# Optimization experiments

Hardware: AMD Instinct MI355X
Metric: run time of the kernel (lower is better)

## Reference

```python
import jax, jax.numpy as jnp
import numpy as np

B, T, D, U = 64, 2048, 128, 256


def setup_inputs() -> dict:
    key = jax.random.key(0)
    k1, k2, k3 = jax.random.split(key, 3)
    inputs = jax.random.normal(k1, (B, T, D), dtype=jnp.float32)
    # kernel: Dense(4*units, use_bias=False) -> Wx [D, 4U]
    Wx = jax.random.normal(k2, (D, 4 * U), dtype=jnp.float32) * (1.0 / np.sqrt(D))
    # recurrent_kernel: Dense(4*units) with bias (orthogonal init approximated by scaled normal)
    Wh = jax.random.normal(k3, (U, 4 * U), dtype=jnp.float32) * (1.0 / np.sqrt(U))
    b = jnp.zeros((4 * U,), dtype=jnp.float32)
    return {"inputs": inputs, "Wx": Wx, "Wh": Wh, "b": b}


def reference(inputs, Wx, Wh, b):
    units = Wh.shape[0]
    batch = inputs.shape[0]
    # Precompute input projections for all timesteps: [B, T, 4U]
    xz = jnp.einsum('btd,dk->btk', inputs, Wx)

    def step(carry, xz_t):
        h, c = carry
        z = xz_t + h @ Wh + b  # [B, 4U]
        zi, zf, zg, zo = jnp.split(z, 4, axis=-1)
        i = jax.nn.sigmoid(zi)
        f = jax.nn.sigmoid(zf)
        o = jax.nn.sigmoid(zo)
        c_new = f * c + i * jnp.tanh(zg)
        h_new = o * jnp.tanh(c_new)
        return (h_new, c_new), h_new

    h0 = jnp.zeros((batch, units), dtype=inputs.dtype)
    c0 = jnp.zeros((batch, units), dtype=inputs.dtype)
    # scan over time: xz transposed to [T, B, 4U]
    _, hs = jax.lax.scan(step, (h0, c0), jnp.swapaxes(xz, 0, 1))
    return jnp.swapaxes(hs, 0, 1)  # [B, T, U]
```

## Files before the change

### kernel.cpp

```cpp
#include <hip/hip_runtime.h>
#include <hip/hip_fp16.h>


#define NB 64
#define NT 2048
#define ND 128
#define NU 256
#define N4U 1024

#define WREG 96
#define WLDS 32

typedef _Float16 f16;
typedef _Float16 f16x2 __attribute__((ext_vector_type(2)));
typedef _Float16 f16x8 __attribute__((ext_vector_type(8)));
typedef float f32x4 __attribute__((ext_vector_type(4)));

__device__ __forceinline__ float dot2(f16x2 a, f16x2 b, float c) {
  return __builtin_amdgcn_fdot2(a, b, c, false);
}

__device__ __forceinline__ float sigm(float x) { return 1.0f / (1.0f + __expf(-x)); }
__device__ __forceinline__ float tanh_(float x) { return 1.0f - 2.0f / (__expf(2.0f * x) + 1.0f); }

__global__ __launch_bounds__(256) void xz_gemm(const float* __restrict__ X,
                                               const float* __restrict__ Wx,
                                               float* __restrict__ XZ,
                                               int t0, int tc) {
  __shared__ __align__(16) float xs[64][ND];
  __shared__ __align__(16) float ws[ND][64];
  const int tid = threadIdx.x;
  const int b = blockIdx.y;
  const int row0 = t0 + blockIdx.x * 64;
  const int col0 = blockIdx.z * 64;

  {
    const float* src = X + ((size_t)b * NT + row0) * ND;
#pragma unroll
    for (int ii = 0; ii < 8; ++ii) {
      int q = tid + 256 * ii;
      int r = q >> 5;
      int k4 = q & 31;
      f32x4 v = *(const f32x4*)(src + (size_t)r * ND + 4 * k4);
      *(f32x4*)&xs[r][4 * k4] = v;
    }
#pragma unroll
    for (int ii = 0; ii < 8; ++ii) {
      int q = tid + 256 * ii;
      int k = q >> 4;
      int c4 = q & 15;
      f32x4 v = *(const f32x4*)(Wx + (size_t)k * N4U + col0 + 4 * c4);
      *(f32x4*)&ws[k][4 * c4] = v;
    }
  }
  __syncthreads();

  const int tx = tid & 15, ty = tid >> 4;
  float acc[4][4];
#pragma unroll
  for (int i = 0; i < 4; ++i)
#pragma unroll
    for (int j = 0; j < 4; ++j) acc[i][j] = 0.0f;

#pragma unroll 8
  for (int k = 0; k < ND; ++k) {
    f32x4 bv = *(const f32x4*)&ws[k][4 * tx];
    float a0 = xs[4 * ty + 0][k];
    float a1 = xs[4 * ty + 1][k];
    float a2 = xs[4 * ty + 2][k];
    float a3 = xs[4 * ty + 3][k];
#pragma unroll
    for (int j = 0; j < 4; ++j) {
      acc[0][j] += a0 * bv[j];
      acc[1][j] += a1 * bv[j];
      acc[2][j] += a2 * bv[j];
      acc[3][j] += a3 * bv[j];
    }
  }

  float* dst = XZ + ((size_t)b * tc + (row0 - t0)) * N4U + col0;
#pragma unroll
  for (int i = 0; i < 4; ++i) {
    f32x4 v;
#pragma unroll
    for (int j = 0; j < 4; ++j) v[j] = acc[i][j];
    *(f32x4*)(dst + (size_t)(4 * ty + i) * N4U + 4 * tx) = v;
  }
}

__global__ __launch_bounds__(512, 1) void lstm_seq(const float* __restrict__ Wh,
                                                   const float* __restrict__ bias,
                                                   const float* __restrict__ XZ,
                                                   float* __restrict__ out,
                                                   float* __restrict__ state,
                                                   int t0, int tc) {
  extern __shared__ f16x8 wl[];
  __shared__ float zbuf[N4U];
  __shared__ __align__(16) f16 hbuf[NU];

  const int t = threadIdx.x;
  const int b = blockIdx.x;
  const int j0 = t, j1 = t + 512;

  const float bj0 = bias[j0];
  const float bj1 = bias[j1];

  f16x2 wr0[WREG], wr1[WREG];
#pragma unroll
  for (int p = 0; p < WREG; ++p) {
    f16x2 w;
    w.x = (f16)Wh[(size_t)(2 * p) * N4U + j0];
    w.y = (f16)Wh[(size_t)(2 * p + 1) * N4U + j0];
    wr0[p] = w;
    w.x = (f16)Wh[(size_t)(2 * p) * N4U + j1];
    w.y = (f16)Wh[(size_t)(2 * p + 1) * N4U + j1];
    wr1[p] = w;
  }
  for (int g = 0; g < WLDS / 4; ++g) {
    f16x8 w0, w1;
#pragma unroll
    for (int q = 0; q < 4; ++q) {
      int k = 2 * (WREG + 4 * g + q);
      w0[2 * q]     = (f16)Wh[(size_t)k * N4U + j0];
      w0[2 * q + 1] = (f16)Wh[(size_t)(k + 1) * N4U + j0];
      w1[2 * q]     = (f16)Wh[(size_t)k * N4U + j1];
      w1[2 * q + 1] = (f16)Wh[(size_t)(k + 1) * N4U + j1];
    }
    wl[(0 * 8 + g) * 512 + t] = w0;
    wl[(1 * 8 + g) * 512 + t] = w1;
  }

  float creg = 0.0f, hreg = 0.0f;
  if (t < NU) {
    if (t0 != 0) {
      hreg = state[(size_t)b * 2 * NU + t];
      creg = state[(size_t)b * 2 * NU + NU + t];
    }
    hbuf[t] = (f16)hreg;
  }
  __syncthreads();

  float xf0 = XZ[((size_t)b * tc) * N4U + j0];
  float xf1 = XZ[((size_t)b * tc) * N4U + j1];

  for (int s = 0; s < tc; ++s) {
    float a0 = xf0 + bj0;
    float a1 = xf1 + bj1;
    if (s + 1 < tc) {
      xf0 = XZ[((size_t)b * tc + s + 1) * N4U + j0];
      xf1 = XZ[((size_t)b * tc + s + 1) * N4U + j1];
    }

    const f16x8* hb8 = (const f16x8*)hbuf;
#pragma unroll
    for (int g = 0; g < WREG / 4; ++g) {
      union { f16x8 v; f16x2 p[4]; } u;
      u.v = hb8[g];
#pragma unroll
      for (int q = 0; q < 4; ++q) {
        a0 = dot2(u.p[q], wr0[4 * g + q], a0);
        a1 = dot2(u.p[q], wr1[4 * g + q], a1);
      }
    }
#pragma unroll
    for (int g = 0; g < WLDS / 4; ++g) {
      union { f16x8 v; f16x2 p[4]; } u;
      u.v = hb8[WREG / 4 + g];
      union { f16x8 v; f16x2 p[4]; } w0;
      union { f16x8 v; f16x2 p[4]; } w1;
      w0.v = wl[(0 * 8 + g) * 512 + t];
      w1.v = wl[(1 * 8 + g) * 512 + t];
#pragma unroll
      for (int q = 0; q < 4; ++q) {
        a0 = dot2(u.p[q], w0.p[q], a0);
        a1 = dot2(u.p[q], w1.p[q], a1);
      }
    }

    zbuf[j0] = a0;
    zbuf[j1] = a1;
    __syncthreads();

    if (t < NU) {
      float zi = zbuf[t];
      float zf = zbuf[t + 256];
      float zg = zbuf[t + 512];
      float zo = zbuf[t + 768];
      float ig = sigm(zi), fg = sigm(zf), og = sigm(zo), gg = tanh_(zg);
      creg = fg * creg + ig * gg;
      hreg = og * tanh_(creg);
      out[((size_t)b * NT + t0 + s) * NU + t] = hreg;
      hbuf[t] = (f16)hreg;
    }
    __syncthreads();
  }

  if (t < NU) {
    state[(size_t)b * 2 * NU + t] = hreg;
    state[(size_t)b * 2 * NU + NU + t] = creg;
  }
}

extern "C" void kernel_launch(void* const* d_in, const int* in_sizes, int n_in,
                              void* d_out, int out_size, void* d_ws, size_t ws_size,
                              hipStream_t stream) {
  const float* inputs = (const float*)d_in[0];
  const float* Wx     = (const float*)d_in[1];
  const float* Wh     = (const float*)d_in[2];
  const float* bias   = (const float*)d_in[3];
  float* out = (float*)d_out;

  const size_t state_bytes = (size_t)NB * 2 * NU * sizeof(float);
  float* state = (float*)d_ws;
  float* xzbuf = (float*)((char*)d_ws + state_bytes);

  size_t avail = (ws_size > state_bytes) ? (ws_size - state_bytes) : 0;
  size_t step_bytes = (size_t)NB * N4U * sizeof(float);
  long tc_l = (long)(avail / step_bytes);
  int tc = (tc_l > NT) ? NT : (int)tc_l;
  tc = (tc / 64) * 64;
  if (tc < 64) tc = 64;

  const int smem = 2 * 8 * 512 * (int)sizeof(f16x8);
  (void)hipFuncSetAttribute((const void*)lstm_seq,
                            hipFuncAttributeMaxDynamicSharedMemorySize, smem);

  for (int t0 = 0; t0 < NT; t0 += tc) {
    int cur = NT - t0;
    if (cur > tc) cur = tc;
    dim3 g1(cur >> 6, NB, 16);
    xz_gemm<<<g1, 256, 0, stream>>>(inputs, Wx, xzbuf, t0, cur);
    lstm_seq<<<NB, 512, smem, stream>>>(Wh, bias, xzbuf, out, state, t0, cur);
  }
}
```

Before: 3.793 ms.

## Use one thread per gate column with 1024-thread blocks in LSTM recurrence

The recurrent kernel now launches 1024 threads per batch row, each owning a single gate column instead of two. The Wh split changes to 184 rows in registers and 72 rows in LDS (9 groups of f16x8). Each thread also alternates between two accumulators to shorten the dot2 dependency chain. This doubles the waves per block to add latency hiding and per-step parallelism, at the cost of tighter register limits (launch bounds 1024) and more threads joining each barrier.

```diff
diff --git a/kernel.cpp b/kernel.cpp
--- a/kernel.cpp
+++ b/kernel.cpp
@@ -8,8 +8,8 @@
 #define NU 256
 #define N4U 1024
 
-#define WREG 96
-#define WLDS 32
+#define WREG 92
+#define WLG 9
 
 typedef _Float16 f16;
 typedef _Float16 f16x2 __attribute__((ext_vector_type(2)));
@@ -88,46 +88,39 @@
   }
 }
 
-__global__ __launch_bounds__(512, 1) void lstm_seq(const float* __restrict__ Wh,
-                                                   const float* __restrict__ bias,
-                                                   const float* __restrict__ XZ,
-                                                   float* __restrict__ out,
-                                                   float* __restrict__ state,
-                                                   int t0, int tc) {
+__global__ __launch_bounds__(1024, 4) void lstm_seq(const float* __restrict__ Wh,
+                                                    const float* __restrict__ bias,
+                                                    const float* __restrict__ XZ,
+                                                    float* __restrict__ out,
+                                                    float* __restrict__ state,
+                                                    int t0, int tc) {
   extern __shared__ f16x8 wl[];
   __shared__ float zbuf[N4U];
   __shared__ __align__(16) f16 hbuf[NU];
 
   const int t = threadIdx.x;
   const int b = blockIdx.x;
-  const int j0 = t, j1 = t + 512;
-
-  const float bj0 = bias[j0];
-  const float bj1 = bias[j1];
-
-  f16x2 wr0[WREG], wr1[WREG];
+
+  const float bj = bias[t];
+
+  f16x2 wr[WREG];
 #pragma unroll
   for (int p = 0; p < WREG; ++p) {
     f16x2 w;
-    w.x = (f16)Wh[(size_t)(2 * p) * N4U + j0];
-    w.y = (f16)Wh[(size_t)(2 * p + 1) * N4U + j0];
-    wr0[p] = w;
-    w.x = (f16)Wh[(size_t)(2 * p) * N4U + j1];
-    w.y = (f16)Wh[(size_t)(2 * p + 1) * N4U + j1];
-    wr1[p] = w;
-  }
-  for (int g = 0; g < WLDS / 4; ++g) {
-    f16x8 w0, w1;
+    w.x = (f16)Wh[(size_t)(2 * p) * N4U + t];
+    w.y = (f16)Wh[(size_t)(2 * p + 1) * N4U + t];
+    wr[p] = w;
+  }
+#pragma unroll
+  for (int g = 0; g < WLG; ++g) {
+    f16x8 w;
 #pragma unroll
     for (int q = 0; q < 4; ++q) {
-      int k = 2 * (WREG + 4 * g + q);
-      w0[2 * q]     = (f16)Wh[(size_t)k * N4U + j0];
-      w0[2 * q + 1] = (f16)Wh[(size_t)(k + 1) * N4U + j0];
-      w1[2 * q]     = (f16)Wh[(size_t)k * N4U + j1];
-      w1[2 * q + 1] = (f16)Wh[(size_t)(k + 1) * N4U + j1];
-    }
-    wl[(0 * 8 + g) * 512 + t] = w0;
-    wl[(1 * 8 + g) * 512 + t] = w1;
+      int p = WREG + 4 * g + q;
+      w[2 * q]     = (f16)Wh[(size_t)(2 * p) * N4U + t];
+      w[2 * q + 1] = (f16)Wh[(size_t)(2 * p + 1) * N4U + t];
+    }
+    wl[g * 1024 + t] = w;
   }
 
   float creg = 0.0f, hreg = 0.0f;
@@ -140,15 +133,13 @@
   }
   __syncthreads();
 
-  float xf0 = XZ[((size_t)b * tc) * N4U + j0];
-  float xf1 = XZ[((size_t)b * tc) * N4U + j1];
+  float xf = XZ[((size_t)b * tc) * N4U + t];
 
   for (int s = 0; s < tc; ++s) {
-    float a0 = xf0 + bj0;
-    float a1 = xf1 + bj1;
+    float a0 = xf + bj;
+    float e0 = 0.0f;
     if (s + 1 < tc) {
-      xf0 = XZ[((size_t)b * tc + s + 1) * N4U + j0];
-      xf1 = XZ[((size_t)b * tc + s + 1) * N4U + j1];
+      xf = XZ[((size_t)b * tc + s + 1) * N4U + t];
     }
 
     const f16x8* hb8 = (const f16x8*)hbuf;
@@ -158,27 +149,25 @@
       u.v = hb8[g];
 #pragma unroll
       for (int q = 0; q < 4; ++q) {
-        a0 = dot2(u.p[q], wr0[4 * g + q], a0);
-        a1 = dot2(u.p[q], wr1[4 * g + q], a1);
+        if (g & 1) e0 = dot2(u.p[q], wr[4 * g + q], e0);
+        else       a0 = dot2(u.p[q], wr[4 * g + q], a0);
       }
     }
 #pragma unroll
-    for (int g = 0; g < WLDS / 4; ++g) {
+    for (int g = 0; g < WLG; ++g) {
       union { f16x8 v; f16x2 p[4]; } u;
+      union { f16x8 v; f16x2 p[4]; } w;
       u.v = hb8[WREG / 4 + g];
-      union { f16x8 v; f16x2 p[4]; } w0;
-      union { f16x8 v; f16x2 p[4]; } w1;
-      w0.v = wl[(0 * 8 + g) * 512 + t];
-      w1.v = wl[(1 * 8 + g) * 512 + t];
+      w.v = wl[g * 1024 + t];
 #pragma unroll
       for (int q = 0; q < 4; ++q) {
-        a0 = dot2(u.p[q], w0.p[q], a0);
-        a1 = dot2(u.p[q], w1.p[q], a1);
+        if (g & 1) e0 = dot2(u.p[q], w.p[q], e0);
+        else       a0 = dot2(u.p[q], w.p[q], a0);
       }
     }
-
-    zbuf[j0] = a0;
-    zbuf[j1] = a1;
+    a0 += e0;
+
+    zbuf[t] = a0;
     __syncthreads();
 
     if (t < NU) {
@@ -221,7 +210,7 @@
   tc = (tc / 64) * 64;
   if (tc < 64) tc = 64;
 
-  const int smem = 2 * 8 * 512 * (int)sizeof(f16x8);
+  const int smem = WLG * 1024 * (int)sizeof(f16x8);
   (void)hipFuncSetAttribute((const void*)lstm_seq,
                             hipFuncAttributeMaxDynamicSharedMemorySize, smem);
 
@@ -230,6 +219,6 @@
     if (cur > tc) cur = tc;
     dim3 g1(cur >> 6, NB, 16);
     xz_gemm<<<g1, 256, 0, stream>>>(inputs, Wx, xzbuf, t0, cur);
-    lstm_seq<<<NB, 512, smem, stream>>>(Wh, bias, xzbuf, out, state, t0, cur);
-  }
-}
+    lstm_seq<<<NB, 1024, smem, stream>>>(Wh, bias, xzbuf, out, state, t0, cur);
+  }
+}
```

Measured after the change: 4.017 ms. +5.9%, slower.
